# Kernel tuning notes

Measured on AMD Instinct MI355X. Metric: run time of the kernel, lower is better.

The kernel has to match this reference:

```python
import jax, jax.numpy as jnp
import numpy as np

N_NODES = 100000
IN_CH = 128
HID = 64
N_EDGES = 1600000
NEG_SLOPE = 0.2


def setup_inputs() -> dict:
    key = jax.random.key(0)
    k1, k2, k3, k4, k5, k6 = jax.random.split(key, 6)
    x = jax.random.normal(k1, (N_NODES, IN_CH), dtype=jnp.float32)
    edge_index = jax.random.randint(k2, (2, N_EDGES), 0, N_NODES, dtype=jnp.int64)
    # Glorot-style init for GATConv params (heads=1)
    s_w = (2.0 / (IN_CH + HID)) ** 0.5
    W = jax.random.normal(k3, (IN_CH, HID), dtype=jnp.float32) * s_w
    s_a = (2.0 / (1 + HID)) ** 0.5
    att_src = jax.random.normal(k4, (HID,), dtype=jnp.float32) * s_a
    att_dst = jax.random.normal(k5, (HID,), dtype=jnp.float32) * s_a
    bias = jnp.zeros((HID,), dtype=jnp.float32)
    return {"x": x, "edge_index": edge_index, "W": W, "att_src": att_src,
            "att_dst": att_dst, "bias": bias}


def reference(x, edge_index, W, att_src, att_dst, bias):
    N = x.shape[0]
    # PyG GATConv default: add self-loops
    loop = jnp.arange(N, dtype=edge_index.dtype)
    src = jnp.concatenate([edge_index[0], loop])  # message source j
    dst = jnp.concatenate([edge_index[1], loop])  # message target i

    h = x @ W                      # [N, HID]
    a_src = h @ att_src            # [N]
    a_dst = h @ att_dst            # [N]

    # per-edge attention logit: LeakyReLU(a_src[j] + a_dst[i])
    e = jax.nn.leaky_relu(a_src[src] + a_dst[dst], NEG_SLOPE)  # [E+N]
    # numerically-stable segment softmax over destination node
    m = jax.ops.segment_max(e, dst, num_segments=N)
    e = jnp.exp(e - m[dst])
    denom = jax.ops.segment_sum(e, dst, num_segments=N)
    alpha = e / (denom[dst] + 1e-16)               # [E+N]

    # scatter-aggregate weighted source features, then bias
    out = jax.ops.segment_sum(alpha[:, None] * h[src], dst, num_segments=N)
    out = out + bias               # [N, HID]
    return out, alpha[:, None]     # alpha shaped [E+N, heads=1]
```

## Files before the change

kernel.cpp:

```cpp
#include <hip/hip_runtime.h>

#define NN 100000
#define IC 128
#define HD 64
#define NEG 0.2f
#define NPB 32
#define NBKT (NN / NPB)
#define CAP 768
#define TILE 4096
#define NIT 8

typedef float f32x4 __attribute__((ext_vector_type(4)));
typedef short s16x8 __attribute__((ext_vector_type(8)));

__device__ __forceinline__ float bf16u_to_f32(unsigned short u) {
  union { unsigned int i; float f; } v;
  v.i = ((unsigned int)u) << 16;
  return v.f;
}

__device__ __forceinline__ unsigned short f32_to_bf16u(float f) {
  union { float f; unsigned int i; } v;
  v.f = f;
  unsigned int b = v.i;
  b += 0x7FFFu + ((b >> 16) & 1u);
  return (unsigned short)(b >> 16);
}

__global__ __launch_bounds__(256) void k_gemm(const float* __restrict__ x,
                                              const float* __restrict__ W,
                                              const float* __restrict__ att_s,
                                              const float* __restrict__ att_d,
                                              unsigned short* __restrict__ hb,
                                              float* __restrict__ as_,
                                              float* __restrict__ ad_,
                                              int* __restrict__ bktcur) {
  __shared__ unsigned short xb[64 * 128];
  __shared__ unsigned short wt[64 * 128];
  const int tid = threadIdx.x;
  const int n0 = blockIdx.x * 64;
  if (tid < 2 && 2 * blockIdx.x + tid < NBKT) bktcur[2 * blockIdx.x + tid] = 0;

  #pragma unroll
  for (int i = 0; i < 8; ++i) {
    int f = i * 256 + tid;
    int r = f >> 5, k0 = (f & 31) << 2;
    float4 v = make_float4(0.f, 0.f, 0.f, 0.f);
    if (n0 + r < NN) v = *(const float4*)&x[(size_t)(n0 + r) * IC + k0];
    ushort4 u;
    u.x = f32_to_bf16u(v.x); u.y = f32_to_bf16u(v.y);
    u.z = f32_to_bf16u(v.z); u.w = f32_to_bf16u(v.w);
    int idx = r * 128 + k0;
    *(ushort4*)&xb[idx ^ ((r & 7) << 3)] = u;
  }
  #pragma unroll
  for (int i = 0; i < 8; ++i) {
    int f = i * 256 + tid;
    int k = f >> 4, c0 = (f & 15) << 2;
    float4 v = *(const float4*)&W[k * HD + c0];
    const float* vf = (const float*)&v;
    #pragma unroll
    for (int j = 0; j < 4; ++j) {
      int c = c0 + j;
      int idx = c * 128 + k;
      wt[idx ^ ((c & 7) << 3)] = f32_to_bf16u(vf[j]);
    }
  }
  __syncthreads();

  const int wv = tid >> 6, lane = tid & 63;
  const int fr = lane & 15;
  const int fq = lane >> 4;
  const int nodeR = wv * 16 + fr;
  f32x4 acc[4] = {};
  #pragma unroll
  for (int kb = 0; kb < 4; ++kb) {
    int ks = kb * 32 + fq * 8;
    int ia = nodeR * 128 + ks;
    s16x8 af = *(s16x8*)&xb[ia ^ ((nodeR & 7) << 3)];
    #pragma unroll
    for (int cg = 0; cg < 4; ++cg) {
      int col = cg * 16 + fr;
      int ib = col * 128 + ks;
      s16x8 bfr = *(s16x8*)&wt[ib ^ ((col & 7) << 3)];
      acc[cg] = __builtin_amdgcn_mfma_f32_16x16x32_bf16(af, bfr, acc[cg], 0, 0, 0);
    }
  }

  float atts[4], attd[4];
  #pragma unroll
  for (int cg = 0; cg < 4; ++cg) {
    atts[cg] = att_s[cg * 16 + fr];
    attd[cg] = att_d[cg * 16 + fr];
  }
  __syncthreads();
  unsigned short* ho = xb;

  #pragma unroll
  for (int j = 0; j < 4; ++j) {
    int nrel = wv * 16 + fq * 4 + j;
    float ps = acc[0][j]*atts[0] + acc[1][j]*atts[1]
             + acc[2][j]*atts[2] + acc[3][j]*atts[3];
    float pd = acc[0][j]*attd[0] + acc[1][j]*attd[1]
             + acc[2][j]*attd[2] + acc[3][j]*attd[3];
    #pragma unroll
    for (int mk = 1; mk < 16; mk <<= 1) {
      ps += __shfl_xor(ps, mk);
      pd += __shfl_xor(pd, mk);
    }
    if (fr == 0 && n0 + nrel < NN) { as_[n0 + nrel] = ps; ad_[n0 + nrel] = pd; }
    #pragma unroll
    for (int cg = 0; cg < 4; ++cg)
      ho[nrel * 72 + cg * 16 + fr] = f32_to_bf16u(acc[cg][j]);
  }
  __syncthreads();

  {
    int node = tid >> 2, ch = (tid & 3) << 4;
    if (n0 + node < NN) {
      ushort4 a0 = *(ushort4*)&ho[node * 72 + ch];
      ushort4 a1 = *(ushort4*)&ho[node * 72 + ch + 4];
      ushort4 a2 = *(ushort4*)&ho[node * 72 + ch + 8];
      ushort4 a3 = *(ushort4*)&ho[node * 72 + ch + 12];
      unsigned short* dst = &hb[(size_t)(n0 + node) * HD + ch];
      *(ushort4*)(dst) = a0;
      *(ushort4*)(dst + 4) = a1;
      *(ushort4*)(dst + 8) = a2;
      *(ushort4*)(dst + 12) = a3;
    }
  }
}

__global__ __launch_bounds__(512) void k_part(const int* __restrict__ ei,
                                              const float* __restrict__ as_,
                                              const float* __restrict__ ad_,
                                              int* __restrict__ bktcur,
                                              int2* __restrict__ bktbuf,
                                              float* __restrict__ p_lin,
                                              int E, int M) {
  __shared__ int lcnt[NBKT];
  __shared__ int gbs[NBKT];
  const int tid = threadIdx.x;
  const int base = blockIdx.x * TILE;

  for (int c = tid; c < NBKT; c += 512) lcnt[c] = 0;
  __syncthreads();

  int pkx[NIT], rb[NIT];
  float tv[NIT];
  #pragma unroll
  for (int i = 0; i < NIT; ++i) {
    int m = base + i * 512 + tid;
    if (m < M) {
      int s, d;
      if (m < E) { s = ei[m]; d = ei[E + m]; }
      else       { s = m - E; d = s; }
      int b = d >> 5;
      pkx[i] = (s << 5) | (d & 31);
      tv[i] = as_[s] + ad_[d];
      int r = atomicAdd(&lcnt[b], 1);
      rb[i] = (b << 12) | r;
    } else rb[i] = -1;
  }
  __syncthreads();

  for (int c = tid; c < NBKT; c += 512) {
    int v = lcnt[c];
    gbs[c] = v ? atomicAdd(&bktcur[c], v) : 0;
  }
  __syncthreads();

  #pragma unroll
  for (int i = 0; i < NIT; ++i) {
    if (rb[i] >= 0) {
      int m = base + i * 512 + tid;
      float t = tv[i];
      t = t > 0.f ? t : NEG * t;
      float p = __expf(t);
      p_lin[m] = p;
      int b = (unsigned)rb[i] >> 12, r = rb[i] & 4095;
      int slot = gbs[b] + r;
      if (slot < CAP)
        bktbuf[(size_t)b * CAP + slot] = make_int2(pkx[i], __float_as_int(p));
    }
  }
}

__global__ __launch_bounds__(256) void k_pg(const int* __restrict__ bktcur,
                                            const int2* __restrict__ bktbuf,
                                            const unsigned short* __restrict__ hb,
                                            const float* __restrict__ bias,
                                            float* __restrict__ out,
                                            float* __restrict__ denom) {
  __shared__ int2 sp[CAP];
  __shared__ int cnt2[NPB], nstart[NPB], cur[NPB];
  __shared__ float dls[NPB];
  const int b = blockIdx.x;
  const int d0 = b << 5;
  const int tid = threadIdx.x;
  const int cnt = min(bktcur[b], CAP);
  const int2* mybuf = bktbuf + (size_t)b * CAP;
  const char* hbb = (const char*)hb;

  if (tid < NPB) cnt2[tid] = 0;
  __syncthreads();
  for (int e = tid; e < cnt; e += 256) atomicAdd(&cnt2[mybuf[e].x & 31], 1);
  __syncthreads();

  if (tid < 32) {
    int a = cnt2[tid];
    int va = a;
    #pragma unroll
    for (int off = 1; off < 32; off <<= 1) {
      int na = __shfl_up(va, off);
      if (tid >= off) va += na;
    }
    nstart[tid] = va - a;
    cur[tid] = va - a;
  }
  __syncthreads();
  for (int e = tid; e < cnt; e += 256) {
    int2 v = mybuf[e];
    int slot = atomicAdd(&cur[v.x & 31], 1);
    sp[slot] = make_int2((v.x & ~31) << 2, v.y);
  }
  __syncthreads();

  const int wv = tid >> 6, lane = tid & 63;
  const int half = lane >> 5;
  const int hl = lane & 31;
  const unsigned chb = (unsigned)hl << 2;
  const float2 bs2 = *(const float2*)&bias[2 * hl];

  for (int n = wv; n < NPB; n += 4) {
    int beg = nstart[n], end = beg + cnt2[n];
    float ax = 0.f, ay = 0.f, dens = 0.f;
    int e = beg;
    for (; e + 8 <= end; e += 8) {
      #pragma unroll
      for (int j = 0; j < 4; ++j) {
        int2 v = sp[e + 2 * j + half];
        unsigned u = *(const unsigned*)(hbb + ((unsigned)v.x + chb));
        float p = __int_as_float(v.y);
        dens += p;
        ax += p * __uint_as_float(u << 16);
        ay += p * __uint_as_float(u & 0xffff0000u);
      }
    }
    {
      #pragma unroll
      for (int j = 0; j < 4; ++j) {
        int idx = e + 2 * j + half;
        if (idx < end) {
          int2 v = sp[idx];
          unsigned u = *(const unsigned*)(hbb + ((unsigned)v.x + chb));
          float p = __int_as_float(v.y);
          dens += p;
          ax += p * __uint_as_float(u << 16);
          ay += p * __uint_as_float(u & 0xffff0000u);
        }
      }
    }
    ax += __shfl_xor(ax, 32);
    ay += __shfl_xor(ay, 32);
    dens += __shfl_xor(dens, 32);
    if (half == 0) {
      float rd = 1.f / (dens + 1e-16f);
      float2 o;
      o.x = ax * rd + bs2.x;
      o.y = ay * rd + bs2.y;
      *(float2*)&out[(size_t)(d0 + n) * HD + 2 * hl] = o;
      if (hl == 0) dls[n] = dens;
    }
  }
  __syncthreads();
  if (tid < NPB) denom[d0 + tid] = dls[tid];
}

__global__ __launch_bounds__(256) void k_alpha(const int* __restrict__ ei,
                                               const float* __restrict__ p_lin,
                                               const float* __restrict__ denom,
                                               float* __restrict__ alpha_out,
                                               int E, int M) {
  int m = blockIdx.x * 256 + threadIdx.x;
  if (m >= M) return;
  int d = (m < E) ? ei[E + m] : (m - E);
  alpha_out[m] = p_lin[m] / (denom[d] + 1e-16f);
}

extern "C" void kernel_launch(void* const* d_in, const int* in_sizes, int n_in,
                              void* d_out, int out_size, void* d_ws, size_t ws_size,
                              hipStream_t stream) {
  const float* x     = (const float*)d_in[0];
  const int*   ei    = (const int*)d_in[1];
  const float* W     = (const float*)d_in[2];
  const float* att_s = (const float*)d_in[3];
  const float* att_d = (const float*)d_in[4];
  const float* bias  = (const float*)d_in[5];

  const int E = in_sizes[1] / 2;
  const int M = E + NN;

  float* out       = (float*)d_out;
  float* alpha_out = out + (size_t)NN * HD;

  char* w = (char*)d_ws;
  auto alloc = [&](size_t bytes) {
    char* p = w;
    w += (bytes + 15) & ~(size_t)15;
    return p;
  };
  unsigned short* hb = (unsigned short*)alloc(sizeof(unsigned short) * (size_t)NN * HD);
  float* as_    = (float*)alloc(sizeof(float) * NN);
  float* ad_    = (float*)alloc(sizeof(float) * NN);
  float* denom  = (float*)alloc(sizeof(float) * NN);
  float* p_lin  = (float*)alloc(sizeof(float) * (size_t)M);
  int*   bktcur = (int*)alloc(sizeof(int) * NBKT);
  int2*  bktbuf = (int2*)alloc(sizeof(int2) * (size_t)NBKT * CAP);

  k_gemm<<<(NN + 63) / 64, 256, 0, stream>>>(x, W, att_s, att_d, hb, as_, ad_,
                                             bktcur);
  k_part<<<(M + TILE - 1) / TILE, 512, 0, stream>>>(ei, as_, ad_, bktcur,
                                                    bktbuf, p_lin, E, M);
  k_pg<<<NBKT, 256, 0, stream>>>(bktcur, bktbuf, hb, bias, out, denom);
  k_alpha<<<(M + 255) / 256, 256, 0, stream>>>(ei, p_lin, denom, alpha_out,
                                               E, M);
}
```

Baseline: 108.7 us.

## Recompute edge exp logits downstream instead of storing p_lin and packed pairs

The partition kernel now writes only a packed (src,dst-lane) word per edge into the bucket buffer, using one global atomic per edge. It no longer does per-block shared-memory counting or stores exp values. The gather kernel recomputes the exp logit from as_/ad_ while building its per-node lists, and the alpha kernel recomputes it again from edge indices instead of reading p_lin. This removes the p_lin array and halves bucket-buffer traffic, at the cost of extra random as_/ad_ gathers, duplicated exp work, and heavy contention on global bucket counters.

```diff
diff --git a/kernel.cpp b/kernel.cpp
--- a/kernel.cpp
+++ b/kernel.cpp
@@ -7,8 +7,6 @@
 #define NPB 32
 #define NBKT (NN / NPB)
 #define CAP 768
-#define TILE 4096
-#define NIT 8
 
 typedef float f32x4 __attribute__((ext_vector_type(4)));
 typedef short s16x8 __attribute__((ext_vector_type(8)));
@@ -131,80 +129,41 @@
   }
 }
 
-__global__ __launch_bounds__(512) void k_part(const int* __restrict__ ei,
-                                              const float* __restrict__ as_,
-                                              const float* __restrict__ ad_,
+__global__ __launch_bounds__(256) void k_part(const int* __restrict__ ei,
                                               int* __restrict__ bktcur,
-                                              int2* __restrict__ bktbuf,
-                                              float* __restrict__ p_lin,
+                                              unsigned* __restrict__ bktbuf,
                                               int E, int M) {
-  __shared__ int lcnt[NBKT];
-  __shared__ int gbs[NBKT];
-  const int tid = threadIdx.x;
-  const int base = blockIdx.x * TILE;
-
-  for (int c = tid; c < NBKT; c += 512) lcnt[c] = 0;
-  __syncthreads();
-
-  int pkx[NIT], rb[NIT];
-  float tv[NIT];
-  #pragma unroll
-  for (int i = 0; i < NIT; ++i) {
-    int m = base + i * 512 + tid;
-    if (m < M) {
-      int s, d;
-      if (m < E) { s = ei[m]; d = ei[E + m]; }
-      else       { s = m - E; d = s; }
-      int b = d >> 5;
-      pkx[i] = (s << 5) | (d & 31);
-      tv[i] = as_[s] + ad_[d];
-      int r = atomicAdd(&lcnt[b], 1);
-      rb[i] = (b << 12) | r;
-    } else rb[i] = -1;
-  }
-  __syncthreads();
-
-  for (int c = tid; c < NBKT; c += 512) {
-    int v = lcnt[c];
-    gbs[c] = v ? atomicAdd(&bktcur[c], v) : 0;
-  }
-  __syncthreads();
-
-  #pragma unroll
-  for (int i = 0; i < NIT; ++i) {
-    if (rb[i] >= 0) {
-      int m = base + i * 512 + tid;
-      float t = tv[i];
-      t = t > 0.f ? t : NEG * t;
-      float p = __expf(t);
-      p_lin[m] = p;
-      int b = (unsigned)rb[i] >> 12, r = rb[i] & 4095;
-      int slot = gbs[b] + r;
-      if (slot < CAP)
-        bktbuf[(size_t)b * CAP + slot] = make_int2(pkx[i], __float_as_int(p));
-    }
-  }
+  int m = blockIdx.x * 256 + threadIdx.x;
+  if (m >= M) return;
+  int s, d;
+  if (m < E) { s = ei[m]; d = ei[E + m]; }
+  else       { s = m - E; d = s; }
+  int b = d >> 5;
+  int slot = atomicAdd(&bktcur[b], 1);
+  if (slot < CAP) bktbuf[(size_t)b * CAP + slot] = ((unsigned)s << 5) | (d & 31);
 }
 
 __global__ __launch_bounds__(256) void k_pg(const int* __restrict__ bktcur,
-                                            const int2* __restrict__ bktbuf,
+                                            const unsigned* __restrict__ bktbuf,
+                                            const float* __restrict__ as_,
+                                            const float* __restrict__ ad_,
                                             const unsigned short* __restrict__ hb,
                                             const float* __restrict__ bias,
                                             float* __restrict__ out,
                                             float* __restrict__ denom) {
   __shared__ int2 sp[CAP];
   __shared__ int cnt2[NPB], nstart[NPB], cur[NPB];
-  __shared__ float dls[NPB];
+  __shared__ float dls[NPB], adl[NPB];
   const int b = blockIdx.x;
   const int d0 = b << 5;
   const int tid = threadIdx.x;
   const int cnt = min(bktcur[b], CAP);
-  const int2* mybuf = bktbuf + (size_t)b * CAP;
+  const unsigned* mybuf = bktbuf + (size_t)b * CAP;
   const char* hbb = (const char*)hb;
 
-  if (tid < NPB) cnt2[tid] = 0;
-  __syncthreads();
-  for (int e = tid; e < cnt; e += 256) atomicAdd(&cnt2[mybuf[e].x & 31], 1);
+  if (tid < NPB) { cnt2[tid] = 0; adl[tid] = ad_[d0 + tid]; }
+  __syncthreads();
+  for (int e = tid; e < cnt; e += 256) atomicAdd(&cnt2[mybuf[e] & 31], 1);
   __syncthreads();
 
   if (tid < 32) {
@@ -220,9 +179,13 @@
   }
   __syncthreads();
   for (int e = tid; e < cnt; e += 256) {
-    int2 v = mybuf[e];
-    int slot = atomicAdd(&cur[v.x & 31], 1);
-    sp[slot] = make_int2((v.x & ~31) << 2, v.y);
+    unsigned v = mybuf[e];
+    int node = v & 31;
+    float t = as_[v >> 5] + adl[node];
+    t = t > 0.f ? t : NEG * t;
+    float p = __expf(t);
+    int slot = atomicAdd(&cur[node], 1);
+    sp[slot] = make_int2((int)((v & ~31u) << 2), __float_as_int(p));
   }
   __syncthreads();
 
@@ -278,14 +241,19 @@
 }
 
 __global__ __launch_bounds__(256) void k_alpha(const int* __restrict__ ei,
-                                               const float* __restrict__ p_lin,
+                                               const float* __restrict__ as_,
+                                               const float* __restrict__ ad_,
                                                const float* __restrict__ denom,
                                                float* __restrict__ alpha_out,
                                                int E, int M) {
   int m = blockIdx.x * 256 + threadIdx.x;
   if (m >= M) return;
-  int d = (m < E) ? ei[E + m] : (m - E);
-  alpha_out[m] = p_lin[m] / (denom[d] + 1e-16f);
+  int s, d;
+  if (m < E) { s = ei[m]; d = ei[E + m]; }
+  else       { s = m - E; d = s; }
+  float e = as_[s] + ad_[d];
+  e = e > 0.f ? e : NEG * e;
+  alpha_out[m] = __expf(e) / (denom[d] + 1e-16f);
 }
 
 extern "C" void kernel_launch(void* const* d_in, const int* in_sizes, int n_in,
@@ -311,18 +279,16 @@
     return p;
   };
   unsigned short* hb = (unsigned short*)alloc(sizeof(unsigned short) * (size_t)NN * HD);
-  float* as_    = (float*)alloc(sizeof(float) * NN);
-  float* ad_    = (float*)alloc(sizeof(float) * NN);
-  float* denom  = (float*)alloc(sizeof(float) * NN);
-  float* p_lin  = (float*)alloc(sizeof(float) * (size_t)M);
-  int*   bktcur = (int*)alloc(sizeof(int) * NBKT);
-  int2*  bktbuf = (int2*)alloc(sizeof(int2) * (size_t)NBKT * CAP);
+  float*    as_    = (float*)alloc(sizeof(float) * NN);
+  float*    ad_    = (float*)alloc(sizeof(float) * NN);
+  float*    denom  = (float*)alloc(sizeof(float) * NN);
+  int*      bktcur = (int*)alloc(sizeof(int) * NBKT);
+  unsigned* bktbuf = (unsigned*)alloc(sizeof(unsigned) * (size_t)NBKT * CAP);
 
   k_gemm<<<(NN + 63) / 64, 256, 0, stream>>>(x, W, att_s, att_d, hb, as_, ad_,
                                              bktcur);
-  k_part<<<(M + TILE - 1) / TILE, 512, 0, stream>>>(ei, as_, ad_, bktcur,
-                                                    bktbuf, p_lin, E, M);
-  k_pg<<<NBKT, 256, 0, stream>>>(bktcur, bktbuf, hb, bias, out, denom);
-  k_alpha<<<(M + 255) / 256, 256, 0, stream>>>(ei, p_lin, denom, alpha_out,
+  k_part<<<(M + 255) / 256, 256, 0, stream>>>(ei, bktcur, bktbuf, E, M);
+  k_pg<<<NBKT, 256, 0, stream>>>(bktcur, bktbuf, as_, ad_, hb, bias, out, denom);
+  k_alpha<<<(M + 255) / 256, 256, 0, stream>>>(ei, as_, ad_, denom, alpha_out,
                                                E, M);
 }
```

Result: slower. 255.7 us (+135.2%).
